# Kernel tuning notes

Hardware: AMD Instinct MI355X
Metric: run time of the kernel (lower is better)

Reference implementation:

```python
import jax, jax.numpy as jnp
from jax import lax
import numpy as np

PATCH = 10
DT_RANK = 32
D_STATE = 16

def silu(x):
    return x * jax.nn.sigmoid(x)

def layernorm(x, g, b, eps=1e-5):
    m = jnp.mean(x, -1, keepdims=True)
    v = jnp.var(x, -1, keepdims=True)
    return (x - m) * lax.rsqrt(v + eps) * g + b

def causal_dwconv(x, w, b):
    # x: (B,L,D), w: (D,K) depthwise, b: (D,). Torch pad=K-1 then [:L] == causal left pad.
    D, K = w.shape
    y = lax.conv_general_dilated(x.transpose(0, 2, 1), w[:, None, :], (1,), [(K - 1, 0)],
                                 feature_group_count=D,
                                 dimension_numbers=('NCH', 'OIH', 'NCH'))
    return y.transpose(0, 2, 1) + b

def selective_scan(u, delta, A, Bm, C, Dp):
    # u,delta:(B,L,D)  A:(D,N)  Bm,C:(B,L,N)  Dp:(D,)
    dA = jnp.exp(delta[..., None] * A)                          # (B,L,D,N)
    dBu = delta[..., None] * Bm[:, :, None, :] * u[..., None]   # (B,L,D,N)
    h0 = jnp.zeros((u.shape[0],) + A.shape, u.dtype)            # (B,D,N)
    def step(h, inp):
        dA_t, dBu_t, C_t = inp
        h = dA_t * h + dBu_t
        return h, jnp.einsum('bdn,bn->bd', h, C_t)
    _, ys = lax.scan(step, h0, (dA.swapaxes(0, 1), dBu.swapaxes(0, 1), C.swapaxes(0, 1)))
    return ys.swapaxes(0, 1) + u * Dp

def mamba(x, p):
    # Mamba(d_model=512, d_state=16, d_conv=4, expand=1)
    xm, z = jnp.split(x @ p['in'].swapaxes(-1, -2), 2, -1)
    xm = silu(causal_dwconv(xm, p['cw'], p['cb']))
    dt, Bm, C = jnp.split(xm @ p['xp'].swapaxes(-1, -2), [DT_RANK, DT_RANK + D_STATE], -1)
    delta = jax.nn.softplus(dt @ p['dtw'].swapaxes(-1, -2) + p['dtb'])
    A = -jnp.exp(p['Al'])
    y = selective_scan(xm, delta, A, Bm, C, p['D'])
    return (y * silu(z)) @ p['ow'].swapaxes(-1, -2)

def block(x, p):
    xn = layernorm(x, p['ln_g'], p['ln_b'])
    xc, res = jnp.split(xn @ p['in_w'].swapaxes(-1, -2), 2, -1)
    xc = silu(causal_dwconv(xc, p['cw'], p['cb']))
    yf = mamba(xc, p['mf'])
    yb = jnp.flip(mamba(jnp.flip(xc, 1), p['mb']), 1)
    gate = silu(res)  # broadcast gate over both directions (cat halves)
    y = jnp.concatenate([yf * gate, yb * gate], -1)
    return y @ p['out_w'].swapaxes(-1, -2) + x

def forward(x, patch_w, patch_b, cls_token, ln_g, ln_b, in_w, cw, cb,
            mf_in, mf_cw, mf_cb, mf_xp, mf_dtw, mf_dtb, mf_Al, mf_D, mf_ow,
            mb_in, mb_cw, mb_cb, mb_xp, mb_dtw, mb_dtb, mb_Al, mb_D, mb_ow,
            out_w, fn_g, fn_b):
    B = x.shape[0]
    h = lax.conv_general_dilated(x, patch_w, (PATCH,), 'VALID',
                                 dimension_numbers=('NCH', 'OIH', 'NCH'))
    h = h.transpose(0, 2, 1) + patch_b                    # (B, P, 256)
    cls = jnp.broadcast_to(cls_token, (B, 1, cls_token.shape[-1]))
    h = jnp.concatenate([cls, h], 1)                      # (B, P+1, 256)
    stacked = {'ln_g': ln_g, 'ln_b': ln_b, 'in_w': in_w, 'cw': cw, 'cb': cb, 'out_w': out_w,
               'mf': {'in': mf_in, 'cw': mf_cw, 'cb': mf_cb, 'xp': mf_xp, 'dtw': mf_dtw,
                      'dtb': mf_dtb, 'Al': mf_Al, 'D': mf_D, 'ow': mf_ow},
               'mb': {'in': mb_in, 'cw': mb_cw, 'cb': mb_cb, 'xp': mb_xp, 'dtw': mb_dtw,
                      'dtb': mb_dtb, 'Al': mb_Al, 'D': mb_D, 'ow': mb_ow}}
    h, _ = lax.scan(lambda c, p: (block(c, p), None), h, stacked)
    h = layernorm(h, fn_g, fn_b)
    return h[:, 0]

def setup_inputs():
    key = jax.random.key(0)
    ks = iter(jax.random.split(key, 64))
    def rn(shape, scale=1.0):
        return jax.random.normal(next(ks), shape, jnp.float32) * scale
    L, di, n, r = 8, 512, D_STATE, DT_RANK
    inp = {
        'x': rn((4, 129, 5000)),
        'patch_w': rn((256, 129, 10), (129 * 10) ** -0.5),
        'patch_b': rn((256,), 0.02),
        'cls_token': rn((1, 1, 256)),
        'ln_g': jnp.ones((L, 256)), 'ln_b': jnp.zeros((L, 256)),
        'in_w': rn((L, 1024, 256), 256 ** -0.5),
        'cw': rn((L, 512, 4), 0.5), 'cb': rn((L, 512), 0.02),
        'out_w': rn((L, 256, 1024), 1024 ** -0.5),
        'fn_g': jnp.ones((256,)), 'fn_b': jnp.zeros((256,)),
    }
    for pre in ('mf', 'mb'):
        inp[pre + '_in'] = rn((L, 2 * di, di), di ** -0.5)
        inp[pre + '_cw'] = rn((L, di, 4), 0.5)
        inp[pre + '_cb'] = rn((L, di), 0.02)
        inp[pre + '_xp'] = rn((L, r + 2 * n, di), di ** -0.5)
        inp[pre + '_dtw'] = rn((L, di, r), r ** -0.5)
        inp[pre + '_dtb'] = rn((L, di), 0.5)
        inp[pre + '_Al'] = jax.random.uniform(next(ks), (L, di, n), jnp.float32)
        inp[pre + '_D'] = jnp.ones((L, di))
        inp[pre + '_ow'] = rn((L, di, di), di ** -0.5)
    return inp

def reference(x, patch_w, patch_b, cls_token, ln_g, ln_b, in_w, cw, cb,
              mf_in, mf_cw, mf_cb, mf_xp, mf_dtw, mf_dtb, mf_Al, mf_D, mf_ow,
              mb_in, mb_cw, mb_cb, mb_xp, mb_dtw, mb_dtb, mb_Al, mb_D, mb_ow,
              out_w, fn_g, fn_b):
    return forward(x, patch_w, patch_b, cls_token, ln_g, ln_b, in_w, cw, cb,
                   mf_in, mf_cw, mf_cb, mf_xp, mf_dtw, mf_dtb, mf_Al, mf_D, mf_ow,
                   mb_in, mb_cw, mb_cb, mb_xp, mb_dtw, mb_dtb, mb_Al, mb_D, mb_ow,
                   out_w, fn_g, fn_b)
```

## Files before the change

### kernel.cpp

```cpp
#include <hip/hip_runtime.h>
#include <math.h>

constexpr int B   = 4;
constexpr int S   = 501;
constexpr int T   = B * S;
constexpr int DM  = 256;
constexpr int DI  = 512;
constexpr int DH  = 1024;
constexpr int NST = 16;
constexpr int RDT = 32;
constexpr int LAYERS = 8;

constexpr int CS     = 16;
constexpr int NCH    = (S + CS - 1) / CS;
constexpr int NSTATE = 2 * B * DI * NST;

constexpr long WSEG1 = 262144;
constexpr long WSEG2 = WSEG1 + 524288;
constexpr long WSEG3 = WSEG2 + 524288;
constexpr long WSEG4 = WSEG3 + 262144;
constexpr long WSEG5 = WSEG4 + 262144;
constexpr long WSEGT = WSEG5 + 262144;

constexpr int PK = 1312;

typedef __attribute__((ext_vector_type(8))) short bf16x8;
typedef __attribute__((ext_vector_type(4))) short bf16x4;
typedef __attribute__((ext_vector_type(4))) float f32x4;

__device__ __forceinline__ float silu_f(float x) { return x / (1.0f + expf(-x)); }
__device__ __forceinline__ float softplus_f(float x) { return x > 20.0f ? x : log1pf(expf(x)); }

__device__ __forceinline__ unsigned short f2bf(float f) {
    unsigned u = __float_as_uint(f);
    u += 0x7FFF + ((u >> 16) & 1);
    return (unsigned short)(u >> 16);
}
__device__ __forceinline__ float bf2f(unsigned short s) {
    return __uint_as_float((unsigned)s << 16);
}
__device__ __forceinline__ void splitf(float x, unsigned short& h, unsigned short& l) {
    h = f2bf(x);
    l = f2bf(x - bf2f(h));
}

__global__ __launch_bounds__(256)
void lsplit_k(const float* __restrict__ s0, const float* __restrict__ s1,
              const float* __restrict__ s2, const float* __restrict__ s3,
              const float* __restrict__ s4, const float* __restrict__ s5,
              unsigned short* __restrict__ hi, unsigned short* __restrict__ lo)
{
    long i = ((long)blockIdx.x * 256 + threadIdx.x) * 8;
    const float* src; long off;
    if      (i < WSEG1) { src = s0; off = 0; }
    else if (i < WSEG2) { src = s1; off = WSEG1; }
    else if (i < WSEG3) { src = s2; off = WSEG2; }
    else if (i < WSEG4) { src = s3; off = WSEG3; }
    else if (i < WSEG5) { src = s4; off = WSEG4; }
    else                { src = s5; off = WSEG5; }
    const float* p = src + (i - off);
    float4 a = ((const float4*)p)[0];
    float4 b4 = ((const float4*)p)[1];
    float v[8] = {a.x, a.y, a.z, a.w, b4.x, b4.y, b4.z, b4.w};
    unsigned short h8[8], l8[8];
#pragma unroll
    for (int j = 0; j < 8; ++j) splitf(v[j], h8[j], l8[j]);
    *(bf16x8*)(hi + i) = *(const bf16x8*)h8;
    *(bf16x8*)(lo + i) = *(const bf16x8*)l8;
}

__global__ __launch_bounds__(256)
void pwsplit_k(const float* __restrict__ pw, unsigned short* __restrict__ hi,
               unsigned short* __restrict__ lo)
{
    long i = ((long)blockIdx.x * 256 + threadIdx.x) * 8;
    int row = (int)(i / PK);
    int col = (int)(i - (long)row * PK);
    unsigned short h8[8], l8[8];
#pragma unroll
    for (int j = 0; j < 8; ++j) {
        int cc = col + j;
        float v = (cc < 1290) ? pw[(long)row * 1290 + cc] : 0.0f;
        splitf(v, h8[j], l8[j]);
    }
    *(bf16x8*)(hi + i) = *(const bf16x8*)h8;
    *(bf16x8*)(lo + i) = *(const bf16x8*)l8;
}

__global__ __launch_bounds__(256, 2)
void pgemm_k(const float* __restrict__ x, const unsigned short* __restrict__ PWh,
             const unsigned short* __restrict__ PWl, const float* __restrict__ pb,
             float* __restrict__ h)
{
    constexpr int LDAs = 40;
    __shared__ unsigned short sm[4 * 64 * LDAs];
    unsigned short* Ah_s = sm;
    unsigned short* Al_s = sm + 64 * LDAs;
    unsigned short* Wh_s = sm + 2 * 64 * LDAs;
    unsigned short* Wl_s = sm + 3 * 64 * LDAs;

    const int tid = threadIdx.x;
    const int lane = tid & 63;
    const int wave = tid >> 6;
    const int wr = wave >> 1, wc = wave & 1;
    const int m0 = blockIdx.x * 64, n0 = blockIdx.y * 64;
    const int kl = lane >> 4, rl = lane & 15;

    const int arow = tid >> 2, acs = (tid & 3) * 8;
    const int m = m0 + arow;
    const bool mok = m < 2000;
    const int bq = m / 500, tp = m - bq * 500;
    const float* xb = x + (long)bq * 129 * 5000 + tp * 10;

    f32x4 acc[2][2];
#pragma unroll
    for (int i = 0; i < 2; ++i)
#pragma unroll
        for (int j = 0; j < 2; ++j) acc[i][j] = (f32x4){0.f, 0.f, 0.f, 0.f};

    for (int k0 = 0; k0 < PK; k0 += 32) {
        unsigned short ah8[8], al8[8];
#pragma unroll
        for (int e = 0; e < 8; ++e) {
            int kk = k0 + acs + e;
            int c = kk / 10, kq = kk - c * 10;
            float v = (mok && kk < 1290) ? xb[(long)c * 5000 + kq] : 0.0f;
            splitf(v, ah8[e], al8[e]);
        }
        *(bf16x8*)(Ah_s + arow * LDAs + acs) = *(const bf16x8*)ah8;
        *(bf16x8*)(Al_s + arow * LDAs + acs) = *(const bf16x8*)al8;
        {
            long gi = (long)(n0 + arow) * PK + k0 + acs;
            *(bf16x8*)(Wh_s + arow * LDAs + acs) = *(const bf16x8*)(PWh + gi);
            *(bf16x8*)(Wl_s + arow * LDAs + acs) = *(const bf16x8*)(PWl + gi);
        }
        __syncthreads();

        bf16x8 ah[2], al[2], wh[2], wl[2];
#pragma unroll
        for (int i = 0; i < 2; ++i) {
            int r = wr * 32 + i * 16 + rl;
            ah[i] = *(const bf16x8*)&Ah_s[r * LDAs + kl * 8];
            al[i] = *(const bf16x8*)&Al_s[r * LDAs + kl * 8];
        }
#pragma unroll
        for (int j = 0; j < 2; ++j) {
            int r = wc * 32 + j * 16 + rl;
            wh[j] = *(const bf16x8*)&Wh_s[r * LDAs + kl * 8];
            wl[j] = *(const bf16x8*)&Wl_s[r * LDAs + kl * 8];
        }
#pragma unroll
        for (int i = 0; i < 2; ++i)
#pragma unroll
            for (int j = 0; j < 2; ++j) {
                acc[i][j] = __builtin_amdgcn_mfma_f32_16x16x32_bf16(ah[i], wl[j], acc[i][j], 0, 0, 0);
                acc[i][j] = __builtin_amdgcn_mfma_f32_16x16x32_bf16(al[i], wh[j], acc[i][j], 0, 0, 0);
                acc[i][j] = __builtin_amdgcn_mfma_f32_16x16x32_bf16(ah[i], wh[j], acc[i][j], 0, 0, 0);
            }
        __syncthreads();
    }

#pragma unroll
    for (int i = 0; i < 2; ++i)
#pragma unroll
        for (int j = 0; j < 2; ++j) {
            int colg = n0 + wc * 32 + j * 16 + (lane & 15);
            float bias = pb[colg];
            int rbase = m0 + wr * 32 + i * 16 + (lane >> 4) * 4;
#pragma unroll
            for (int r = 0; r < 4; ++r) {
                int mm = rbase + r;
                if (mm >= 2000) continue;
                int bb = mm / 500, tt = mm - bb * 500;
                h[(long)(bb * 501 + 1 + tt) * DM + colg] = acc[i][j][r] + bias;
            }
        }
}

__global__ __launch_bounds__(64)
void cls_k(const float* __restrict__ cls, float* __restrict__ h)
{
    int b = blockIdx.x, lane = threadIdx.x;
    ((float4*)(h + (long)b * S * DM))[lane] = ((const float4*)cls)[lane];
}

template<bool SPLIT>
__global__ __launch_bounds__(64)
void ln_k(const float* __restrict__ hin, const float* __restrict__ g,
          const float* __restrict__ be, float* __restrict__ outf,
          unsigned short* __restrict__ oh, unsigned short* __restrict__ ol, int rowMul)
{
    long hr = (long)blockIdx.x * rowMul;
    int lane = threadIdx.x;
    float4 v = ((const float4*)(hin + hr * DM))[lane];
    float s = v.x + v.y + v.z + v.w;
    float q = v.x * v.x + v.y * v.y + v.z * v.z + v.w * v.w;
#pragma unroll
    for (int off = 32; off; off >>= 1) { s += __shfl_xor(s, off); q += __shfl_xor(q, off); }
    float mean = s * (1.0f / DM);
    float var  = q * (1.0f / DM) - mean * mean;
    float rs = rsqrtf(var + 1e-5f);
    float4 gg = ((const float4*)g)[lane];
    float4 bb = ((const float4*)be)[lane];
    float o[4];
    o[0] = (v.x - mean) * rs * gg.x + bb.x;
    o[1] = (v.y - mean) * rs * gg.y + bb.y;
    o[2] = (v.z - mean) * rs * gg.z + bb.z;
    o[3] = (v.w - mean) * rs * gg.w + bb.w;
    if constexpr (SPLIT) {
        unsigned short h4[4], l4[4];
#pragma unroll
        for (int j = 0; j < 4; ++j) splitf(o[j], h4[j], l4[j]);
        long idx = (long)blockIdx.x * DM + lane * 4;
        *(bf16x4*)(oh + idx) = *(const bf16x4*)h4;
        *(bf16x4*)(ol + idx) = *(const bf16x4*)l4;
    } else {
        ((float4*)(outf + (long)blockIdx.x * DM))[lane] = make_float4(o[0], o[1], o[2], o[3]);
    }
}

template<int BM, int BN, int EPI>
__global__ __launch_bounds__(256, 2)
void mgemm_k(const unsigned short* __restrict__ Ah0, const unsigned short* __restrict__ Al0,
             const unsigned short* __restrict__ Ah1, const unsigned short* __restrict__ Al1,
             int lda,
             const unsigned short* __restrict__ Wh0, const unsigned short* __restrict__ Wl0,
             const unsigned short* __restrict__ Wh1, const unsigned short* __restrict__ Wl1,
             float* __restrict__ Cout, long cStrideZ, int ldc,
             const float* __restrict__ resid,
             unsigned short* __restrict__ Oh, unsigned short* __restrict__ Ol,
             int M, int N, int K)
{
    constexpr int MI = BM / 32;
    constexpr int NJ = BN / 32;
    constexpr int LDAs = 40;

    __shared__ unsigned short sm[(2 * BM + 2 * BN) * LDAs];
    unsigned short* Ah_s = sm;
    unsigned short* Al_s = sm + BM * LDAs;
    unsigned short* Wh_s = sm + 2 * BM * LDAs;
    unsigned short* Wl_s = sm + 2 * BM * LDAs + BN * LDAs;

    const int dir = blockIdx.z;
    const unsigned short* __restrict__ A_h = dir ? Ah1 : Ah0;
    const unsigned short* __restrict__ A_l = dir ? Al1 : Al0;
    const unsigned short* __restrict__ W_h = dir ? Wh1 : Wh0;
    const unsigned short* __restrict__ W_l = dir ? Wl1 : Wl0;
    const int tid = threadIdx.x;
    const int lane = tid & 63;
    const int wave = tid >> 6;
    const int wr = wave >> 1, wc = wave & 1;
    const int m0 = blockIdx.x * BM, n0 = blockIdx.y * BN;
    const int kl = lane >> 4, rl = lane & 15;

    f32x4 acc[MI][NJ];
#pragma unroll
    for (int i = 0; i < MI; ++i)
#pragma unroll
        for (int j = 0; j < NJ; ++j) acc[i][j] = (f32x4){0.f, 0.f, 0.f, 0.f};

    const bf16x8 zv = {0, 0, 0, 0, 0, 0, 0, 0};

    for (int k0 = 0; k0 < K; k0 += 32) {
        if constexpr (BM == 128) {
            int row = tid >> 1, cs = (tid & 1) * 16;
            {
                bool ok = (m0 + row) < M;
                long gi = (long)(m0 + row) * lda + k0 + cs;
                bf16x8 h0 = zv, h1 = zv, l0 = zv, l1 = zv;
                if (ok) {
                    h0 = *(const bf16x8*)(A_h + gi);
                    h1 = *(const bf16x8*)(A_h + gi + 8);
                    l0 = *(const bf16x8*)(A_l + gi);
                    l1 = *(const bf16x8*)(A_l + gi + 8);
                }
                *(bf16x8*)(Ah_s + row * LDAs + cs) = h0;
                *(bf16x8*)(Ah_s + row * LDAs + cs + 8) = h1;
                *(bf16x8*)(Al_s + row * LDAs + cs) = l0;
                *(bf16x8*)(Al_s + row * LDAs + cs + 8) = l1;
            }
            {
                long gi = (long)(n0 + row) * K + k0 + cs;
                *(bf16x8*)(Wh_s + row * LDAs + cs)     = *(const bf16x8*)(W_h + gi);
                *(bf16x8*)(Wh_s + row * LDAs + cs + 8) = *(const bf16x8*)(W_h + gi + 8);
                *(bf16x8*)(Wl_s + row * LDAs + cs)     = *(const bf16x8*)(W_l + gi);
                *(bf16x8*)(Wl_s + row * LDAs + cs + 8) = *(const bf16x8*)(W_l + gi + 8);
            }
        } else {
            int t2 = tid & 127;
            int row = t2 >> 1, cs = (t2 & 1) * 16;
            if (tid < 128) {
                bool ok = (m0 + row) < M;
                long gi = (long)(m0 + row) * lda + k0 + cs;
                bf16x8 h0 = zv, h1 = zv, l0 = zv, l1 = zv;
                if (ok) {
                    h0 = *(const bf16x8*)(A_h + gi);
                    h1 = *(const bf16x8*)(A_h + gi + 8);
                    l0 = *(const bf16x8*)(A_l + gi);
                    l1 = *(const bf16x8*)(A_l + gi + 8);
                }
                *(bf16x8*)(Ah_s + row * LDAs + cs) = h0;
                *(bf16x8*)(Ah_s + row * LDAs + cs + 8) = h1;
                *(bf16x8*)(Al_s + row * LDAs + cs) = l0;
                *(bf16x8*)(Al_s + row * LDAs + cs + 8) = l1;
            } else {
                long gi = (long)(n0 + row) * K + k0 + cs;
                *(bf16x8*)(Wh_s + row * LDAs + cs)     = *(const bf16x8*)(W_h + gi);
                *(bf16x8*)(Wh_s + row * LDAs + cs + 8) = *(const bf16x8*)(W_h + gi + 8);
                *(bf16x8*)(Wl_s + row * LDAs + cs)     = *(const bf16x8*)(W_l + gi);
                *(bf16x8*)(Wl_s + row * LDAs + cs + 8) = *(const bf16x8*)(W_l + gi + 8);
            }
        }
        __syncthreads();

        bf16x8 ah[MI], al[MI], wh[NJ], wl[NJ];
#pragma unroll
        for (int i = 0; i < MI; ++i) {
            int r = wr * (BM / 2) + i * 16 + rl;
            ah[i] = *(const bf16x8*)&Ah_s[r * LDAs + kl * 8];
            al[i] = *(const bf16x8*)&Al_s[r * LDAs + kl * 8];
        }
#pragma unroll
        for (int j = 0; j < NJ; ++j) {
            int r = wc * (BN / 2) + j * 16 + rl;
            wh[j] = *(const bf16x8*)&Wh_s[r * LDAs + kl * 8];
            wl[j] = *(const bf16x8*)&Wl_s[r * LDAs + kl * 8];
        }
#pragma unroll
        for (int i = 0; i < MI; ++i)
#pragma unroll
            for (int j = 0; j < NJ; ++j) {
                acc[i][j] = __builtin_amdgcn_mfma_f32_16x16x32_bf16(ah[i], wl[j], acc[i][j], 0, 0, 0);
                acc[i][j] = __builtin_amdgcn_mfma_f32_16x16x32_bf16(al[i], wh[j], acc[i][j], 0, 0, 0);
                acc[i][j] = __builtin_amdgcn_mfma_f32_16x16x32_bf16(ah[i], wh[j], acc[i][j], 0, 0, 0);
            }
        __syncthreads();
    }

    float* C = Cout + (long)dir * cStrideZ;
#pragma unroll
    for (int i = 0; i < MI; ++i) {
#pragma unroll
        for (int j = 0; j < NJ; ++j) {
            int rbase = m0 + wr * (BM / 2) + i * 16 + (lane >> 4) * 4;
            int colg = n0 + wc * (BN / 2) + j * 16 + (lane & 15);
#pragma unroll
            for (int r = 0; r < 4; ++r) {
                int rowg = rbase + r;
                if (rowg >= M) continue;
                float val = acc[i][j][r];
                if constexpr (EPI == 0) {
                    C[(long)rowg * ldc + colg] = val;
                } else if constexpr (EPI == 2) {
                    int bb = rowg / S;
                    int t  = rowg - bb * S;
                    long rt = dir ? (long)(bb * S + (S - 1 - t)) : (long)rowg;
                    float g = resid[rt * DH + DI + colg];
                    float o = val * silu_f(g);
                    unsigned short hh, ll;
                    splitf(o, hh, ll);
                    Oh[rt * DH + (dir ? DI : 0) + colg] = hh;
                    Ol[rt * DH + (dir ? DI : 0) + colg] = ll;
                } else {
                    C[(long)rowg * ldc + colg] = val + resid[(long)rowg * ldc + colg];
                }
            }
        }
    }
}

template<int EPI>
__global__ __launch_bounds__(256)
void gemm_k(const float* __restrict__ A0, const float* __restrict__ A1, int lda,
            const float* __restrict__ W0, const float* __restrict__ W1,
            const float* __restrict__ b0, const float* __restrict__ b1,
            float* __restrict__ Cout, long cStrideZ, int ldc,
            int M, int N, int K)
{
    const int dir = blockIdx.z;
    const float* __restrict__ A = dir ? A1 : A0;
    const float* __restrict__ W = dir ? W1 : W0;
    __shared__ float As[16][64];
    __shared__ float Ws[16][64];
    const int tid = threadIdx.x;
    const int tx = tid & 15, ty = tid >> 4;
    const int m0 = blockIdx.x * 64, n0 = blockIdx.y * 64;
    const int arow = tid >> 2;
    const int acol = (tid & 3) * 4;
    float acc[4][4] = {};

    for (int k0 = 0; k0 < K; k0 += 16) {
        {
            int row = m0 + arow;
            float4 va = make_float4(0.f, 0.f, 0.f, 0.f);
            if (row < M) va = *(const float4*)(A + (long)row * lda + k0 + acol);
            As[acol + 0][arow] = va.x; As[acol + 1][arow] = va.y;
            As[acol + 2][arow] = va.z; As[acol + 3][arow] = va.w;
            float4 vw = *(const float4*)(W + (long)(n0 + arow) * K + k0 + acol);
            Ws[acol + 0][arow] = vw.x; Ws[acol + 1][arow] = vw.y;
            Ws[acol + 2][arow] = vw.z; Ws[acol + 3][arow] = vw.w;
        }
        __syncthreads();
#pragma unroll
        for (int kk = 0; kk < 16; ++kk) {
            float4 av = *(const float4*)&As[kk][ty * 4];
            float4 wv = *(const float4*)&Ws[kk][tx * 4];
            float a[4] = {av.x, av.y, av.z, av.w};
            float w[4] = {wv.x, wv.y, wv.z, wv.w};
#pragma unroll
            for (int i = 0; i < 4; ++i)
#pragma unroll
                for (int j = 0; j < 4; ++j)
                    acc[i][j] = fmaf(a[i], w[j], acc[i][j]);
        }
        __syncthreads();
    }

    const float* bias = dir ? b1 : b0;
    float* C = Cout + (long)dir * cStrideZ;
#pragma unroll
    for (int i = 0; i < 4; ++i) {
        int row = m0 + ty * 4 + i;
        if (row >= M) continue;
        int col = n0 + tx * 4;
        if constexpr (EPI == 0) {
            float4 v = make_float4(acc[i][0], acc[i][1], acc[i][2], acc[i][3]);
            *(float4*)(C + (long)row * ldc + col) = v;
        } else {
            float4 b4 = *(const float4*)(bias + col);
            float4 v;
            v.x = softplus_f(acc[i][0] + b4.x);
            v.y = softplus_f(acc[i][1] + b4.y);
            v.z = softplus_f(acc[i][2] + b4.z);
            v.w = softplus_f(acc[i][3] + b4.w);
            *(float4*)(C + (long)row * ldc + col) = v;
        }
    }
}

template<int MODE>
__global__ __launch_bounds__(256)
void conv_k(const float* __restrict__ in0, const float* __restrict__ in1,
            const float* __restrict__ cw0, const float* __restrict__ cw1,
            const float* __restrict__ cb0, const float* __restrict__ cb1,
            float* __restrict__ outf, long outStrideZ,
            unsigned short* __restrict__ oh, unsigned short* __restrict__ ol,
            unsigned short* __restrict__ orh, unsigned short* __restrict__ orl)
{
    const int dir = blockIdx.z;
    const float* __restrict__ in = dir ? in1 : in0;
    const float* __restrict__ cw = dir ? cw1 : cw0;
    const float* __restrict__ cb = dir ? cb1 : cb0;
    int idx = blockIdx.x * 256 + threadIdx.x;
    if (idx >= T * DI) return;
    int d = idx & (DI - 1);
    int r = idx >> 9;
    int b = r / S, t = r - b * S;
    float acc = cb[d];
#pragma unroll
    for (int k = 0; k < 4; ++k) {
        int tt = t - 3 + k;
        if (tt >= 0) acc = fmaf(cw[d * 4 + k], in[(long)(b * S + tt) * DH + d], acc);
    }
    acc = silu_f(acc);
    if constexpr (MODE == 0) {
        unsigned short hh, ll;
        splitf(acc, hh, ll);
        long i0 = (long)r * DI + d;
        long i1 = (long)(b * S + (S - 1 - t)) * DI + d;
        oh[i0] = hh;  ol[i0] = ll;
        orh[i1] = hh; orl[i1] = ll;
    } else {
        (outf + (long)dir * outStrideZ)[(long)r * DI + d] = acc;
    }
}

__global__ __launch_bounds__(512)
void scanA_k(const float* __restrict__ delta, const float* __restrict__ dtBC,
             const float* __restrict__ u,
             const float* __restrict__ Al0, const float* __restrict__ Al1,
             float* __restrict__ Pb, float* __restrict__ Qb)
{
    __shared__ float B_s[CS * 16];
    const int b = blockIdx.x, c = blockIdx.y, dir = blockIdx.z;
    const int d = threadIdx.x;
    const int c0 = c * CS;
    const int tt = min(CS, S - c0);

    const float* dl  = delta + (long)dir * T * DI + (long)b * S * DI;
    const float* bcp = dtBC  + (long)dir * T * 64 + (long)b * S * 64;
    const float* uu  = u     + (long)dir * T * DI + (long)b * S * DI;

    if (threadIdx.x < CS * 16) {
        int t = threadIdx.x >> 4, n = threadIdx.x & 15;
        B_s[threadIdx.x] = (t < tt) ? bcp[(long)(c0 + t) * 64 + RDT + n] : 0.f;
    }
    __syncthreads();

    const float* Al = dir ? Al1 : Al0;
    float A2[16], Pv[16], Qv[16];
#pragma unroll
    for (int i = 0; i < 4; ++i) {
        float4 a4 = *(const float4*)(Al + (long)d * NST + 4 * i);
        A2[4 * i + 0] = -__expf(a4.x);
        A2[4 * i + 1] = -__expf(a4.y);
        A2[4 * i + 2] = -__expf(a4.z);
        A2[4 * i + 3] = -__expf(a4.w);
    }
#pragma unroll
    for (int n = 0; n < 16; ++n) { Pv[n] = 1.0f; Qv[n] = 0.0f; }

#pragma unroll 2
    for (int t = 0; t < tt; ++t) {
        float dv = dl[(long)(c0 + t) * DI + d];
        float uv = uu[(long)(c0 + t) * DI + d];
        float dvu = dv * uv;
#pragma unroll
        for (int n = 0; n < 16; ++n) {
            float a = __expf(dv * A2[n]);
            Pv[n] *= a;
            Qv[n] = fmaf(a, Qv[n], dvu * B_s[t * 16 + n]);
        }
    }

    long st0 = ((long)(dir * B + b) * DI + d) * NST;
    long co  = (long)c * NSTATE;
#pragma unroll
    for (int i = 0; i < 4; ++i) {
        *(float4*)(Pb + co + st0 + 4 * i) =
            make_float4(Pv[4 * i], Pv[4 * i + 1], Pv[4 * i + 2], Pv[4 * i + 3]);
        *(float4*)(Qb + co + st0 + 4 * i) =
            make_float4(Qv[4 * i], Qv[4 * i + 1], Qv[4 * i + 2], Qv[4 * i + 3]);
    }
}

__global__ __launch_bounds__(256)
void scanB_k(const float* __restrict__ Pb, const float* __restrict__ Qb,
             float* __restrict__ h0)
{
    const int st = blockIdx.x * 256 + threadIdx.x;
    float Pv[NCH], Qv[NCH];
#pragma unroll
    for (int c = 0; c < NCH; ++c) {
        Pv[c] = Pb[(long)c * NSTATE + st];
        Qv[c] = Qb[(long)c * NSTATE + st];
    }
    float h = 0.0f;
#pragma unroll
    for (int c = 0; c < NCH; ++c) {
        h0[(long)c * NSTATE + st] = h;
        h = fmaf(Pv[c], h, Qv[c]);
    }
}

__global__ __launch_bounds__(512)
void scanC_k(const float* __restrict__ delta, const float* __restrict__ dtBC,
             const float* __restrict__ u, const float* __restrict__ xmz,
             const float* __restrict__ Al0, const float* __restrict__ Al1,
             const float* __restrict__ D0, const float* __restrict__ D1,
             const float* __restrict__ h0,
             unsigned short* __restrict__ ph, unsigned short* __restrict__ pl)
{
    __shared__ float BC_s[CS * 32];
    const int b = blockIdx.x, c = blockIdx.y, dir = blockIdx.z;
    const int d = threadIdx.x;
    const int c0 = c * CS;
    const int tt = min(CS, S - c0);

    const float* dl  = delta + (long)dir * T * DI + (long)b * S * DI;
    const float* bcp = dtBC  + (long)dir * T * 64 + (long)b * S * 64;
    const float* uu  = u     + (long)dir * T * DI + (long)b * S * DI;
    const float* zz  = xmz   + (long)dir * T * DH + (long)b * S * DH + DI;
    unsigned short* poh = ph + (long)dir * T * DI + (long)b * S * DI;
    unsigned short* pol = pl + (long)dir * T * DI + (long)b * S * DI;

    {
        int t = threadIdx.x >> 5, j = threadIdx.x & 31;
        BC_s[threadIdx.x] = (t < tt) ? bcp[(long)(c0 + t) * 64 + RDT + j] : 0.f;
    }
    __syncthreads();

    const float* Al = dir ? Al1 : Al0;
    float A2[16], hv[16];
#pragma unroll
    for (int i = 0; i < 4; ++i) {
        float4 a4 = *(const float4*)(Al + (long)d * NST + 4 * i);
        A2[4 * i + 0] = -__expf(a4.x);
        A2[4 * i + 1] = -__expf(a4.y);
        A2[4 * i + 2] = -__expf(a4.z);
        A2[4 * i + 3] = -__expf(a4.w);
    }
    long st0 = ((long)(dir * B + b) * DI + d) * NST;
#pragma unroll
    for (int i = 0; i < 4; ++i) {
        float4 h4 = *(const float4*)(h0 + (long)c * NSTATE + st0 + 4 * i);
        hv[4 * i + 0] = h4.x; hv[4 * i + 1] = h4.y;
        hv[4 * i + 2] = h4.z; hv[4 * i + 3] = h4.w;
    }
    const float Dp = (dir ? D1 : D0)[d];

#pragma unroll 2
    for (int t = 0; t < tt; ++t) {
        float dv = dl[(long)(c0 + t) * DI + d];
        float uv = uu[(long)(c0 + t) * DI + d];
        float zv = zz[(long)(c0 + t) * DH + d];
        float dvu = dv * uv;
        float y = 0.0f;
#pragma unroll
        for (int n = 0; n < 16; ++n) {
            float a = __expf(dv * A2[n]);
            hv[n] = fmaf(a, hv[n], dvu * BC_s[t * 32 + n]);
            y = fmaf(hv[n], BC_s[t * 32 + 16 + n], y);
        }
        float sz = zv / (1.0f + __expf(-zv));
        float o = (y + uv * Dp) * sz;
        unsigned short hh, ll;
        splitf(o, hh, ll);
        poh[(long)(c0 + t) * DI + d] = hh;
        pol[(long)(c0 + t) * DI + d] = ll;
    }
}

extern "C" void kernel_launch(void* const* d_in, const int* in_sizes, int n_in,
                              void* d_out, int out_size, void* d_ws, size_t ws_size,
                              hipStream_t stream)
{
    (void)in_sizes; (void)n_in; (void)out_size; (void)ws_size;
    const float* x        = (const float*)d_in[0];
    const float* patch_w  = (const float*)d_in[1];
    const float* patch_b  = (const float*)d_in[2];
    const float* cls_tok  = (const float*)d_in[3];
    const float* ln_g     = (const float*)d_in[4];
    const float* ln_b     = (const float*)d_in[5];
    const float* in_w     = (const float*)d_in[6];
    const float* cw       = (const float*)d_in[7];
    const float* cb       = (const float*)d_in[8];
    const float* out_w    = (const float*)d_in[9];
    const float* fn_g     = (const float*)d_in[10];
    const float* fn_b     = (const float*)d_in[11];
    const float* mf_in    = (const float*)d_in[12];
    const float* mf_cw    = (const float*)d_in[13];
    const float* mf_cb    = (const float*)d_in[14];
    const float* mf_xp    = (const float*)d_in[15];
    const float* mf_dtw   = (const float*)d_in[16];
    const float* mf_dtb   = (const float*)d_in[17];
    const float* mf_Al    = (const float*)d_in[18];
    const float* mf_D     = (const float*)d_in[19];
    const float* mf_ow    = (const float*)d_in[20];
    const float* mb_in    = (const float*)d_in[21];
    const float* mb_cw    = (const float*)d_in[22];
    const float* mb_cb    = (const float*)d_in[23];
    const float* mb_xp    = (const float*)d_in[24];
    const float* mb_dtw   = (const float*)d_in[25];
    const float* mb_dtb   = (const float*)d_in[26];
    const float* mb_Al    = (const float*)d_in[27];
    const float* mb_D     = (const float*)d_in[28];
    const float* mb_ow    = (const float*)d_in[29];

    float* ws = (float*)d_ws;
    float* h      = ws;
    float* xcres  = h     + (long)T * DM;
    float* xmz    = xcres + (long)T * DH;
    float* u      = xmz   + 2L * T * DH;
    float* dtBC   = u     + 2L * T * DI;
    float* delta  = dtBC  + 2L * T * 64;
    float* Pb     = delta + 2L * T * DI;
    float* Qb     = Pb    + (long)NCH * NSTATE;
    float* h0b    = Qb    + (long)NCH * NSTATE;
    unsigned short* us = (unsigned short*)(h0b + (long)NCH * NSTATE);
    unsigned short* xnh  = us;
    unsigned short* xnl  = xnh + (long)T * DM;
    unsigned short* xch  = xnl + (long)T * DM;
    unsigned short* xcl  = xch + (long)T * DI;
    unsigned short* xrvh = xcl + (long)T * DI;
    unsigned short* xrvl = xrvh + (long)T * DI;
    unsigned short* ph   = xrvl + (long)T * DI;
    unsigned short* pl   = ph   + 2L * T * DI;
    unsigned short* ych  = pl   + 2L * T * DI;
    unsigned short* ycl  = ych  + (long)T * DH;
    unsigned short* WH   = ycl  + (long)T * DH;
    unsigned short* WL   = WH   + WSEGT;
    unsigned short* PWH  = WL   + WSEGT;
    unsigned short* PWL  = PWH  + 256L * PK;

    const long o_inw = 0, o_fin = WSEG1, o_bin = WSEG2, o_fow = WSEG3,
               o_bow = WSEG4, o_oww = WSEG5;

    pwsplit_k<<<dim3(256 * PK / 2048), 256, 0, stream>>>(patch_w, PWH, PWL);
    pgemm_k<<<dim3(32, 4), 256, 0, stream>>>(x, PWH, PWL, patch_b, h);
    cls_k<<<dim3(B), 64, 0, stream>>>(cls_tok, h);

    constexpr int GM64  = (T + 63) / 64;
    constexpr int GM128 = (T + 127) / 128;

    for (int l = 0; l < LAYERS; ++l) {
        const float* lng = ln_g + (long)l * DM;
        const float* lnb = ln_b + (long)l * DM;
        const float* inw = in_w + (long)l * DH * DM;
        const float* cwl = cw   + (long)l * DI * 4;
        const float* cbl = cb   + (long)l * DI;
        const float* oww = out_w + (long)l * DM * DH;
        const float* fin = mf_in + (long)l * DH * DI;
        const float* bin = mb_in + (long)l * DH * DI;
        const float* fcw = mf_cw + (long)l * DI * 4;
        const float* bcw = mb_cw + (long)l * DI * 4;
        const float* fcb = mf_cb + (long)l * DI;
        const float* bcb = mb_cb + (long)l * DI;
        const float* fxp = mf_xp + (long)l * (RDT + 2 * NST) * DI;
        const float* bxp = mb_xp + (long)l * (RDT + 2 * NST) * DI;
        const float* fdw = mf_dtw + (long)l * DI * RDT;
        const float* bdw = mb_dtw + (long)l * DI * RDT;
        const float* fdb = mf_dtb + (long)l * DI;
        const float* bdb = mb_dtb + (long)l * DI;
        const float* fAl = mf_Al + (long)l * DI * NST;
        const float* bAl = mb_Al + (long)l * DI * NST;
        const float* fD  = mf_D  + (long)l * DI;
        const float* bD  = mb_D  + (long)l * DI;
        const float* fow = mf_ow + (long)l * DI * DI;
        const float* bow = mb_ow + (long)l * DI * DI;

        lsplit_k<<<dim3(WSEGT / 2048), 256, 0, stream>>>(inw, fin, bin, fow, bow, oww, WH, WL);

        ln_k<true><<<dim3(T), 64, 0, stream>>>(h, lng, lnb, nullptr, xnh, xnl, 1);
        mgemm_k<128, 128, 0><<<dim3(GM128, DH / 128, 1), 256, 0, stream>>>(
            xnh, xnl, xnh, xnl, DM, WH + o_inw, WL + o_inw, WH + o_inw, WL + o_inw,
            xcres, 0, DH, nullptr, nullptr, nullptr, T, DH, DM);
        conv_k<0><<<dim3(T * DI / 256, 1, 1), 256, 0, stream>>>(
            xcres, xcres, cwl, cwl, cbl, cbl, nullptr, 0, xch, xcl, xrvh, xrvl);
        mgemm_k<128, 128, 0><<<dim3(GM128, DH / 128, 2), 256, 0, stream>>>(
            xch, xcl, xrvh, xrvl, DI, WH + o_fin, WL + o_fin, WH + o_bin, WL + o_bin,
            xmz, (long)T * DH, DH, nullptr, nullptr, nullptr, T, DH, DI);
        conv_k<1><<<dim3(T * DI / 256, 1, 2), 256, 0, stream>>>(
            xmz, xmz + (long)T * DH, fcw, bcw, fcb, bcb, u, (long)T * DI,
            nullptr, nullptr, nullptr, nullptr);
        gemm_k<0><<<dim3(GM64, 1, 2), 256, 0, stream>>>(
            u, u + (long)T * DI, DI, fxp, bxp, nullptr, nullptr, dtBC, (long)T * 64, 64,
            T, 64, DI);
        gemm_k<1><<<dim3(GM64, DI / 64, 2), 256, 0, stream>>>(
            dtBC, dtBC + (long)T * 64, 64, fdw, bdw, fdb, bdb, delta, (long)T * DI, DI,
            T, DI, RDT);
        scanA_k<<<dim3(B, NCH, 2), 512, 0, stream>>>(delta, dtBC, u, fAl, bAl, Pb, Qb);
        scanB_k<<<dim3(NSTATE / 256), 256, 0, stream>>>(Pb, Qb, h0b);
        scanC_k<<<dim3(B, NCH, 2), 512, 0, stream>>>(
            delta, dtBC, u, xmz, fAl, bAl, fD, bD, h0b, ph, pl);
        mgemm_k<128, 128, 2><<<dim3(GM128, DI / 128, 2), 256, 0, stream>>>(
            ph, pl, ph + (long)T * DI, pl + (long)T * DI, DI,
            WH + o_fow, WL + o_fow, WH + o_bow, WL + o_bow,
            nullptr, 0, DH, xcres, ych, ycl, T, DI, DI);
        mgemm_k<64, 64, 3><<<dim3(GM64, DM / 64, 1), 256, 0, stream>>>(
            ych, ycl, ych, ycl, DH, WH + o_oww, WL + o_oww, WH + o_oww, WL + o_oww,
            h, 0, DM, h, nullptr, nullptr, T, DM, DH);
    }

    ln_k<false><<<dim3(B), 64, 0, stream>>>(h, fn_g, fn_b, (float*)d_out, nullptr, nullptr, S);
}
```

Baseline: 1.985 ms.

## Shrink GEMM tiles for more blocks, pre-split patch input, reuse generic GEMM

Replaces the dedicated patch-embedding GEMM with a separate kernel that gathers and splits the input patches into bf16 hi/lo arrays, followed by the generic mgemm_k with a new epilogue that writes into the token rows with bias. All per-layer GEMMs switch from 128x128/64x64 tiles to 128x64/64x32, and launch bounds ask for 3-4 blocks per CU, to raise grid size and occupancy. The tile loader is generalized to a strided loop, and a separate weight leading dimension is added. Smaller tiles reduce operand reuse and increase global traffic. The patch path adds an extra pass through memory.

```diff
diff --git a/kernel.cpp b/kernel.cpp
--- a/kernel.cpp
+++ b/kernel.cpp
@@ -23,6 +23,7 @@
 constexpr long WSEGT = WSEG5 + 262144;
 
 constexpr int PK = 1312;
+constexpr int PM = 2000;
 
 typedef __attribute__((ext_vector_type(8))) short bf16x8;
 typedef __attribute__((ext_vector_type(4))) short bf16x4;
@@ -87,94 +88,26 @@
     *(bf16x8*)(lo + i) = *(const bf16x8*)l8;
 }
 
-__global__ __launch_bounds__(256, 2)
-void pgemm_k(const float* __restrict__ x, const unsigned short* __restrict__ PWh,
-             const unsigned short* __restrict__ PWl, const float* __restrict__ pb,
-             float* __restrict__ h)
-{
-    constexpr int LDAs = 40;
-    __shared__ unsigned short sm[4 * 64 * LDAs];
-    unsigned short* Ah_s = sm;
-    unsigned short* Al_s = sm + 64 * LDAs;
-    unsigned short* Wh_s = sm + 2 * 64 * LDAs;
-    unsigned short* Wl_s = sm + 3 * 64 * LDAs;
-
-    const int tid = threadIdx.x;
-    const int lane = tid & 63;
-    const int wave = tid >> 6;
-    const int wr = wave >> 1, wc = wave & 1;
-    const int m0 = blockIdx.x * 64, n0 = blockIdx.y * 64;
-    const int kl = lane >> 4, rl = lane & 15;
-
-    const int arow = tid >> 2, acs = (tid & 3) * 8;
-    const int m = m0 + arow;
-    const bool mok = m < 2000;
-    const int bq = m / 500, tp = m - bq * 500;
-    const float* xb = x + (long)bq * 129 * 5000 + tp * 10;
-
-    f32x4 acc[2][2];
-#pragma unroll
-    for (int i = 0; i < 2; ++i)
-#pragma unroll
-        for (int j = 0; j < 2; ++j) acc[i][j] = (f32x4){0.f, 0.f, 0.f, 0.f};
-
-    for (int k0 = 0; k0 < PK; k0 += 32) {
-        unsigned short ah8[8], al8[8];
-#pragma unroll
-        for (int e = 0; e < 8; ++e) {
-            int kk = k0 + acs + e;
-            int c = kk / 10, kq = kk - c * 10;
-            float v = (mok && kk < 1290) ? xb[(long)c * 5000 + kq] : 0.0f;
-            splitf(v, ah8[e], al8[e]);
-        }
-        *(bf16x8*)(Ah_s + arow * LDAs + acs) = *(const bf16x8*)ah8;
-        *(bf16x8*)(Al_s + arow * LDAs + acs) = *(const bf16x8*)al8;
-        {
-            long gi = (long)(n0 + arow) * PK + k0 + acs;
-            *(bf16x8*)(Wh_s + arow * LDAs + acs) = *(const bf16x8*)(PWh + gi);
-            *(bf16x8*)(Wl_s + arow * LDAs + acs) = *(const bf16x8*)(PWl + gi);
-        }
-        __syncthreads();
-
-        bf16x8 ah[2], al[2], wh[2], wl[2];
-#pragma unroll
-        for (int i = 0; i < 2; ++i) {
-            int r = wr * 32 + i * 16 + rl;
-            ah[i] = *(const bf16x8*)&Ah_s[r * LDAs + kl * 8];
-            al[i] = *(const bf16x8*)&Al_s[r * LDAs + kl * 8];
-        }
-#pragma unroll
-        for (int j = 0; j < 2; ++j) {
-            int r = wc * 32 + j * 16 + rl;
-            wh[j] = *(const bf16x8*)&Wh_s[r * LDAs + kl * 8];
-            wl[j] = *(const bf16x8*)&Wl_s[r * LDAs + kl * 8];
-        }
-#pragma unroll
-        for (int i = 0; i < 2; ++i)
-#pragma unroll
-            for (int j = 0; j < 2; ++j) {
-                acc[i][j] = __builtin_amdgcn_mfma_f32_16x16x32_bf16(ah[i], wl[j], acc[i][j], 0, 0, 0);
-                acc[i][j] = __builtin_amdgcn_mfma_f32_16x16x32_bf16(al[i], wh[j], acc[i][j], 0, 0, 0);
-                acc[i][j] = __builtin_amdgcn_mfma_f32_16x16x32_bf16(ah[i], wh[j], acc[i][j], 0, 0, 0);
-            }
-        __syncthreads();
-    }
-
-#pragma unroll
-    for (int i = 0; i < 2; ++i)
-#pragma unroll
-        for (int j = 0; j < 2; ++j) {
-            int colg = n0 + wc * 32 + j * 16 + (lane & 15);
-            float bias = pb[colg];
-            int rbase = m0 + wr * 32 + i * 16 + (lane >> 4) * 4;
-#pragma unroll
-            for (int r = 0; r < 4; ++r) {
-                int mm = rbase + r;
-                if (mm >= 2000) continue;
-                int bb = mm / 500, tt = mm - bb * 500;
-                h[(long)(bb * 501 + 1 + tt) * DM + colg] = acc[i][j][r] + bias;
-            }
-        }
+__global__ __launch_bounds__(256)
+void xsplit_k(const float* __restrict__ x, unsigned short* __restrict__ xh,
+              unsigned short* __restrict__ xl)
+{
+    int i = blockIdx.x * 256 + threadIdx.x;
+    if (i >= PM * (PK / 8)) return;
+    int m = i / (PK / 8), k8 = i - m * (PK / 8);
+    int b = m / 500, tp = m - b * 500;
+    const float* xb = x + (long)b * 129 * 5000 + tp * 10;
+    unsigned short h8[8], l8[8];
+#pragma unroll
+    for (int e = 0; e < 8; ++e) {
+        int k = k8 * 8 + e;
+        int c = k / 10, kq = k - c * 10;
+        float v = (k < 1290) ? xb[(long)c * 5000 + kq] : 0.0f;
+        splitf(v, h8[e], l8[e]);
+    }
+    long o = (long)m * PK + k8 * 8;
+    *(bf16x8*)(xh + o) = *(const bf16x8*)h8;
+    *(bf16x8*)(xl + o) = *(const bf16x8*)l8;
 }
 
 __global__ __launch_bounds__(64)
@@ -220,12 +153,13 @@
 }
 
 template<int BM, int BN, int EPI>
-__global__ __launch_bounds__(256, 2)
+__global__ __launch_bounds__(256, (BM == 64 ? 4 : 3))
 void mgemm_k(const unsigned short* __restrict__ Ah0, const unsigned short* __restrict__ Al0,
              const unsigned short* __restrict__ Ah1, const unsigned short* __restrict__ Al1,
              int lda,
              const unsigned short* __restrict__ Wh0, const unsigned short* __restrict__ Wl0,
              const unsigned short* __restrict__ Wh1, const unsigned short* __restrict__ Wl1,
+             int ldw,
              float* __restrict__ Cout, long cStrideZ, int ldc,
              const float* __restrict__ resid,
              unsigned short* __restrict__ Oh, unsigned short* __restrict__ Ol,
@@ -234,6 +168,7 @@
     constexpr int MI = BM / 32;
     constexpr int NJ = BN / 32;
     constexpr int LDAs = 40;
+    constexpr int TOT = BM * 2 + BN * 2;
 
     __shared__ unsigned short sm[(2 * BM + 2 * BN) * LDAs];
     unsigned short* Ah_s = sm;
@@ -262,34 +197,10 @@
     const bf16x8 zv = {0, 0, 0, 0, 0, 0, 0, 0};
 
     for (int k0 = 0; k0 < K; k0 += 32) {
-        if constexpr (BM == 128) {
-            int row = tid >> 1, cs = (tid & 1) * 16;
-            {
-                bool ok = (m0 + row) < M;
-                long gi = (long)(m0 + row) * lda + k0 + cs;
-                bf16x8 h0 = zv, h1 = zv, l0 = zv, l1 = zv;
-                if (ok) {
-                    h0 = *(const bf16x8*)(A_h + gi);
-                    h1 = *(const bf16x8*)(A_h + gi + 8);
-                    l0 = *(const bf16x8*)(A_l + gi);
-                    l1 = *(const bf16x8*)(A_l + gi + 8);
-                }
-                *(bf16x8*)(Ah_s + row * LDAs + cs) = h0;
-                *(bf16x8*)(Ah_s + row * LDAs + cs + 8) = h1;
-                *(bf16x8*)(Al_s + row * LDAs + cs) = l0;
-                *(bf16x8*)(Al_s + row * LDAs + cs + 8) = l1;
-            }
-            {
-                long gi = (long)(n0 + row) * K + k0 + cs;
-                *(bf16x8*)(Wh_s + row * LDAs + cs)     = *(const bf16x8*)(W_h + gi);
-                *(bf16x8*)(Wh_s + row * LDAs + cs + 8) = *(const bf16x8*)(W_h + gi + 8);
-                *(bf16x8*)(Wl_s + row * LDAs + cs)     = *(const bf16x8*)(W_l + gi);
-                *(bf16x8*)(Wl_s + row * LDAs + cs + 8) = *(const bf16x8*)(W_l + gi + 8);
-            }
-        } else {
-            int t2 = tid & 127;
-            int row = t2 >> 1, cs = (t2 & 1) * 16;
-            if (tid < 128) {
+#pragma unroll
+        for (int s = tid; s < TOT; s += 256) {
+            if (s < BM * 2) {
+                int row = s >> 1, cs = (s & 1) * 16;
                 bool ok = (m0 + row) < M;
                 long gi = (long)(m0 + row) * lda + k0 + cs;
                 bf16x8 h0 = zv, h1 = zv, l0 = zv, l1 = zv;
@@ -304,7 +215,9 @@
                 *(bf16x8*)(Al_s + row * LDAs + cs) = l0;
                 *(bf16x8*)(Al_s + row * LDAs + cs + 8) = l1;
             } else {
-                long gi = (long)(n0 + row) * K + k0 + cs;
+                int s2 = s - BM * 2;
+                int row = s2 >> 1, cs = (s2 & 1) * 16;
+                long gi = (long)(n0 + row) * ldw + k0 + cs;
                 *(bf16x8*)(Wh_s + row * LDAs + cs)     = *(const bf16x8*)(W_h + gi);
                 *(bf16x8*)(Wh_s + row * LDAs + cs + 8) = *(const bf16x8*)(W_h + gi + 8);
                 *(bf16x8*)(Wl_s + row * LDAs + cs)     = *(const bf16x8*)(W_l + gi);
@@ -361,8 +274,12 @@
                     splitf(o, hh, ll);
                     Oh[rt * DH + (dir ? DI : 0) + colg] = hh;
                     Ol[rt * DH + (dir ? DI : 0) + colg] = ll;
+                } else if constexpr (EPI == 3) {
+                    C[(long)rowg * ldc + colg] = val + resid[(long)rowg * ldc + colg];
                 } else {
-                    C[(long)rowg * ldc + colg] = val + resid[(long)rowg * ldc + colg];
+                    int bb = rowg / 500;
+                    int tt = rowg - bb * 500;
+                    Cout[(long)(bb * S + 1 + tt) * ldc + colg] = val + resid[colg];
                 }
             }
         }
@@ -682,12 +599,17 @@
     unsigned short* WL   = WH   + WSEGT;
     unsigned short* PWH  = WL   + WSEGT;
     unsigned short* PWL  = PWH  + 256L * PK;
+    unsigned short* XTH  = PWL  + 256L * PK;
+    unsigned short* XTL  = XTH  + (long)PM * PK;
 
     const long o_inw = 0, o_fin = WSEG1, o_bin = WSEG2, o_fow = WSEG3,
                o_bow = WSEG4, o_oww = WSEG5;
 
     pwsplit_k<<<dim3(256 * PK / 2048), 256, 0, stream>>>(patch_w, PWH, PWL);
-    pgemm_k<<<dim3(32, 4), 256, 0, stream>>>(x, PWH, PWL, patch_b, h);
+    xsplit_k<<<dim3((PM * (PK / 8) + 255) / 256), 256, 0, stream>>>(x, XTH, XTL);
+    mgemm_k<64, 32, 4><<<dim3((PM + 63) / 64, DM / 32, 1), 256, 0, stream>>>(
+        XTH, XTL, XTH, XTL, PK, PWH, PWL, PWH, PWL, PK,
+        h, 0, DM, patch_b, nullptr, nullptr, PM, DM, PK);
     cls_k<<<dim3(B), 64, 0, stream>>>(cls_tok, h);
 
     constexpr int GM64  = (T + 63) / 64;
@@ -722,13 +644,13 @@
         lsplit_k<<<dim3(WSEGT / 2048), 256, 0, stream>>>(inw, fin, bin, fow, bow, oww, WH, WL);
 
         ln_k<true><<<dim3(T), 64, 0, stream>>>(h, lng, lnb, nullptr, xnh, xnl, 1);
-        mgemm_k<128, 128, 0><<<dim3(GM128, DH / 128, 1), 256, 0, stream>>>(
-            xnh, xnl, xnh, xnl, DM, WH + o_inw, WL + o_inw, WH + o_inw, WL + o_inw,
+        mgemm_k<128, 64, 0><<<dim3(GM128, DH / 64, 1), 256, 0, stream>>>(
+            xnh, xnl, xnh, xnl, DM, WH + o_inw, WL + o_inw, WH + o_inw, WL + o_inw, DM,
             xcres, 0, DH, nullptr, nullptr, nullptr, T, DH, DM);
         conv_k<0><<<dim3(T * DI / 256, 1, 1), 256, 0, stream>>>(
             xcres, xcres, cwl, cwl, cbl, cbl, nullptr, 0, xch, xcl, xrvh, xrvl);
-        mgemm_k<128, 128, 0><<<dim3(GM128, DH / 128, 2), 256, 0, stream>>>(
-            xch, xcl, xrvh, xrvl, DI, WH + o_fin, WL + o_fin, WH + o_bin, WL + o_bin,
+        mgemm_k<128, 64, 0><<<dim3(GM128, DH / 64, 2), 256, 0, stream>>>(
+            xch, xcl, xrvh, xrvl, DI, WH + o_fin, WL + o_fin, WH + o_bin, WL + o_bin, DI,
             xmz, (long)T * DH, DH, nullptr, nullptr, nullptr, T, DH, DI);
         conv_k<1><<<dim3(T * DI / 256, 1, 2), 256, 0, stream>>>(
             xmz, xmz + (long)T * DH, fcw, bcw, fcb, bcb, u, (long)T * DI,
@@ -743,12 +665,12 @@
         scanB_k<<<dim3(NSTATE / 256), 256, 0, stream>>>(Pb, Qb, h0b);
         scanC_k<<<dim3(B, NCH, 2), 512, 0, stream>>>(
             delta, dtBC, u, xmz, fAl, bAl, fD, bD, h0b, ph, pl);
-        mgemm_k<128, 128, 2><<<dim3(GM128, DI / 128, 2), 256, 0, stream>>>(
+        mgemm_k<128, 64, 2><<<dim3(GM128, DI / 64, 2), 256, 0, stream>>>(
             ph, pl, ph + (long)T * DI, pl + (long)T * DI, DI,
-            WH + o_fow, WL + o_fow, WH + o_bow, WL + o_bow,
+            WH + o_fow, WL + o_fow, WH + o_bow, WL + o_bow, DI,
             nullptr, 0, DH, xcres, ych, ycl, T, DI, DI);
-        mgemm_k<64, 64, 3><<<dim3(GM64, DM / 64, 1), 256, 0, stream>>>(
-            ych, ycl, ych, ycl, DH, WH + o_oww, WL + o_oww, WH + o_oww, WL + o_oww,
+        mgemm_k<64, 32, 3><<<dim3(GM64, DM / 32, 1), 256, 0, stream>>>(
+            ych, ycl, ych, ycl, DH, WH + o_oww, WL + o_oww, WH + o_oww, WL + o_oww, DH,
             h, 0, DM, h, nullptr, nullptr, T, DM, DH);
     }
 
```

Measured after the change: 1.831 ms. 1.08x faster.
